# Performance work log

Hardware: AMD Instinct MI355X
Metric: run time of the kernel (lower is better)

Reference implementation:

```python
import jax, jax.numpy as jnp
import numpy as np

D_K = 64
NEG_INF = -1.0e9

def setup_inputs() -> dict:
    key = jax.random.key(0)
    kq, kk, kv, km = jax.random.split(key, 4)
    B, H, S, D = 2, 16, 2048, D_K
    Q = jax.random.normal(kq, (B, H, S, D), dtype=jnp.float32)
    K = jax.random.normal(kk, (B, H, S, D), dtype=jnp.float32)
    V = jax.random.normal(kv, (B, H, S, D), dtype=jnp.float32)
    # True entries are masked out (torch masked_fill semantics)
    attn_mask = jax.random.randint(km, (B, H, S, S), 0, 2).astype(jnp.bool_)
    return {"Q": Q, "K": K, "V": V, "attn_mask": attn_mask}

def reference(Q, K, V, attn_mask):
    # scores: [B, H, len_q, len_k]
    scale = 1.0 / np.sqrt(D_K).astype(np.float32)
    scores = jnp.einsum('bhqd,bhkd->bhqk', Q, K) * scale
    scores = jnp.where(attn_mask, jnp.float32(NEG_INF), scores)
    attn = jax.nn.softmax(scores, axis=-1)
    prob = jnp.einsum('bhqk,bhkd->bhqd', attn, V)
    return (prob, attn)
```

## Files before the change

### kernel.cpp

```cpp
#include <hip/hip_runtime.h>
#include <hip/hip_bf16.h>

#define S_LEN 2048
#define D_DIM 64
#define QT    64
#define KT    64
#define NTHR  256
#define NKT   (S_LEN / KT)
#define NBLK  1024
#define PROB_ELEMS 4194304LL

typedef float        f32x4  __attribute__((ext_vector_type(4)));
typedef int          i32x4  __attribute__((ext_vector_type(4)));
typedef unsigned int u32x4  __attribute__((ext_vector_type(4)));
typedef short        bf16x8 __attribute__((ext_vector_type(8)));

__device__ __forceinline__ unsigned short f2bf(float f) {
    return __builtin_bit_cast(unsigned short, __float2bfloat16(f));
}
__device__ __forceinline__ int swzc(int row, int ch) {
    return ch ^ ((row ^ (row >> 3)) & 7);
}
__device__ __forceinline__ float4 scale4(float4 v, float s) {
    v.x *= s; v.y *= s; v.z *= s; v.w *= s; return v;
}
__device__ __forceinline__ u32x4 packbf(float4 a, float4 b) {
    u32x4 r;
    r[0] = (unsigned)f2bf(a.x) | ((unsigned)f2bf(a.y) << 16);
    r[1] = (unsigned)f2bf(a.z) | ((unsigned)f2bf(a.w) << 16);
    r[2] = (unsigned)f2bf(b.x) | ((unsigned)f2bf(b.y) << 16);
    r[3] = (unsigned)f2bf(b.z) | ((unsigned)f2bf(b.w) << 16);
    return r;
}
__device__ __forceinline__ unsigned cvtpk(float lo, float hi) {
    unsigned r;
    asm("v_cvt_pk_bf16_f32 %0, %1, %2" : "=v"(r) : "v"(lo), "v"(hi));
    return r;
}
__device__ __forceinline__ void glds16(const unsigned* g, unsigned char* l) {
    __builtin_amdgcn_global_load_lds(
        (const __attribute__((address_space(1))) unsigned*)g,
        (__attribute__((address_space(3))) unsigned*)(void*)l, 16, 0, 0);
}
#define BC8(x) __builtin_bit_cast(bf16x8, (x))
#define MFMA(A, B, C) __builtin_amdgcn_mfma_f32_16x16x32_bf16((A), (B), (C), 0, 0, 0)

#define SFENCE() __builtin_amdgcn_sched_barrier(0)
#define WAITBAR(N)                                                          \
    SFENCE();                                                               \
    asm volatile("s_waitcnt vmcnt(" #N ")" ::: "memory");                   \
    SFENCE();                                                               \
    __builtin_amdgcn_s_barrier();                                           \
    SFENCE();

__global__ void mask_probe_kernel(const unsigned int* __restrict__ m,
                                  int* __restrict__ flag) {
    unsigned int v = m[threadIdx.x];
    unsigned long long ok = __ballot(v <= 1u);
    if (threadIdx.x == 0) *flag = (ok == ~0ULL) ? 1 : 0;
}

#define KPART 524288
#define VPART 65536
__global__ __launch_bounds__(256)
void kv_prep(const float* __restrict__ Kg, const float* __restrict__ Vg,
             unsigned* __restrict__ Kbf, unsigned* __restrict__ Vtb) {
    int tid = blockIdx.x * 256 + threadIdx.x;
    if (tid < KPART) {
        int ch = tid & 7, rowg = tid >> 3;
        const float* src = Kg + (long long)rowg * D_DIM + ch * 8;
        float4 a = *(const float4*)src, b = *(const float4*)(src + 4);
        int bh = rowg >> 11, k = rowg & 2047, kt = k >> 6, row = k & 63;
        unsigned* dst = Kbf + ((unsigned)(bh * NKT + kt) << 11)
                            + row * 32 + swzc(row, ch) * 4;
        *(u32x4*)dst = packbf(a, b);
    } else if (tid < KPART + VPART) {
        int idx = tid - KPART;
        int d = idx & 63, kt = (idx >> 6) & 31, bh = idx >> 11;
        const float* vb = Vg + (long long)(bh * S_LEN + kt * KT) * D_DIM + d;
        unsigned* tile = Vtb + ((unsigned)(bh * NKT + kt) << 11) + d * 32;
        #pragma unroll
        for (int ci = 0; ci < 8; ++ci) {
            u32x4 o;
            #pragma unroll
            for (int s = 0; s < 4; ++s) {
                float lo = vb[(ci * 8 + 2 * s) * D_DIM];
                float hi = vb[(ci * 8 + 2 * s + 1) * D_DIM];
                o[s] = (unsigned)f2bf(lo) | ((unsigned)f2bf(hi) << 16);
            }
            *(u32x4*)(tile + swzc(d, ci) * 4) = o;
        }
    }
}

#define GLDS_K(KS, KTV)                                                     \
    { const unsigned* kp_ = Kbf + ktile0 + (unsigned)(KTV) * 2048u;         \
      glds16(kp_ + f0u, (KS) + dst0); glds16(kp_ + f1u, (KS) + dst1); }
#define GLDS_V(VT, KTV)                                                     \
    { const unsigned* vp_ = Vtb + ktile0 + (unsigned)(KTV) * 2048u;         \
      glds16(vp_ + f0u, (VT) + dst0); glds16(vp_ + f1u, (VT) + dst1); }

#define PREF_MASKF(MI4, MU, KTV)                                            \
    { if (mask32) {                                                         \
        _Pragma("unroll")                                                   \
        for (int n_ = 0; n_ < 4; ++n_)                                      \
          MI4[n_] = *(const i32x4*)(maskI + rowoff                          \
                      + (unsigned)((KTV) * KT + n_ * 16 + 4 * g));          \
      } else {                                                              \
        _Pragma("unroll")                                                   \
        for (int n_ = 0; n_ < 4; ++n_)                                      \
          MU[n_] = *(const unsigned*)(maskB + rowoff                        \
                      + (unsigned)((KTV) * KT + n_ * 16 + 4 * g));          \
      } }

#define BITS16F(DST, MI4, MU)                                               \
    { unsigned bz_ = 0u;                                                    \
      if (mask32) {                                                         \
        _Pragma("unroll")                                                   \
        for (int n_ = 0; n_ < 4; ++n_)                                      \
          bz_ |= ((MI4[n_][0] ? 1u : 0u) | (MI4[n_][1] ? 2u : 0u) |         \
                  (MI4[n_][2] ? 4u : 0u) | (MI4[n_][3] ? 8u : 0u)) << (n_ * 4); \
      } else {                                                              \
        _Pragma("unroll")                                                   \
        for (int n_ = 0; n_ < 4; ++n_) { unsigned mb_ = MU[n_];             \
          bz_ |= (((mb_ & 0xffu) ? 1u : 0u) | ((mb_ & 0xff00u) ? 2u : 0u) | \
                  ((mb_ & 0xff0000u) ? 4u : 0u) |                           \
                  ((mb_ & 0xff000000u) ? 8u : 0u)) << (n_ * 4); }           \
      }                                                                     \
      (DST) = bz_; }

#define GLOAD_BITS(DST, KTV)                                                \
    { (DST) = (unsigned)bitsWS[bitbase + (unsigned)(KTV) * NTHR]; }

#define GP1_TILE(KS, BITS)                                                  \
    { unsigned bb = (BITS);                                                 \
      _Pragma("unroll")                                                     \
      for (int n = 0; n < 4; ++n) {                                         \
        int rowk = n * 16 + c;                                              \
        bf16x8 kf0 = *(const bf16x8*)((KS) + rowk * 128 + swzc(rowk, g) * 16);     \
        bf16x8 kf1 = *(const bf16x8*)((KS) + rowk * 128 + swzc(rowk, 4 + g) * 16); \
        f32x4 acc = {0.f, 0.f, 0.f, 0.f};                                   \
        acc = MFMA(kf0, qf0, acc); acc = MFMA(kf1, qf1, acc);               \
        unsigned mb = bb >> (n * 4);                                        \
        psum += (mb & 1u) ? 0.f : __expf(acc[0]);                           \
        psum += (mb & 2u) ? 0.f : __expf(acc[1]);                           \
        psum += (mb & 4u) ? 0.f : __expf(acc[2]);                           \
        psum += (mb & 8u) ? 0.f : __expf(acc[3]);                           \
      } }

#define GP2_TILE(KS, VT, BITS, KTV)                                         \
    { unsigned bb = (BITS);                                                 \
      _Pragma("unroll")                                                     \
      for (int n = 0; n < 4; ++n) {                                         \
        int rowk = n * 16 + c;                                              \
        bf16x8 kf0 = *(const bf16x8*)((KS) + rowk * 128 + swzc(rowk, g) * 16);     \
        bf16x8 kf1 = *(const bf16x8*)((KS) + rowk * 128 + swzc(rowk, 4 + g) * 16); \
        f32x4 acc = {0.f, 0.f, 0.f, 0.f};                                   \
        acc = MFMA(kf0, qf0, acc); acc = MFMA(kf1, qf1, acc);               \
        unsigned mb = bb >> (n * 4);                                        \
        f32x4 ev;                                                           \
        ev[0] = (mb & 1u) ? 0.f : __expf(acc[0]) * rinv;                    \
        ev[1] = (mb & 2u) ? 0.f : __expf(acc[1]) * rinv;                    \
        ev[2] = (mb & 4u) ? 0.f : __expf(acc[2]) * rinv;                    \
        ev[3] = (mb & 8u) ? 0.f : __expf(acc[3]) * rinv;                    \
        unsigned idx0 = rowoff + (unsigned)((KTV) * KT + n * 16 + 4 * g);   \
        *(f32x4*)(attnOut + idx0) = ev;              \
        uint2 pkv; pkv.x = cvtpk(ev[0], ev[1]); pkv.y = cvtpk(ev[2], ev[3]);\
        int kloc = n * 16 + 4 * g;                                          \
        *(uint2*)(Ps + ql * 128 + swzc(ql, kloc >> 3) * 16 + (kloc & 7) * 2) = pkv; \
      }                                                                     \
      { bf16x8 pa0 = *(const bf16x8*)(Ps + ql * 128 + swzc(ql, g) * 16);    \
        bf16x8 pa1 = *(const bf16x8*)(Ps + ql * 128 + swzc(ql, 4 + g) * 16);\
        __builtin_amdgcn_s_setprio(1);                                      \
        _Pragma("unroll")                                                   \
        for (int df = 0; df < 4; ++df) {                                    \
            int d = df * 16 + c;                                            \
            bf16x8 vb0 = *(const bf16x8*)((VT) + d * 128 + swzc(d, g) * 16);     \
            bf16x8 vb1 = *(const bf16x8*)((VT) + d * 128 + swzc(d, 4 + g) * 16); \
            pacc[df] = MFMA(pa0, vb0, pacc[df]);                            \
            pacc[df] = MFMA(pa1, vb1, pacc[df]);                            \
        }                                                                   \
        __builtin_amdgcn_s_setprio(0); } }

__global__ __launch_bounds__(NTHR, 4)
void attn_fused_glds(const float* __restrict__ Qg,
                     const unsigned* __restrict__ Kbf,
                     const unsigned* __restrict__ Vtb,
                     const unsigned char* __restrict__ maskB,
                     const int* __restrict__ flagp,
                     unsigned short* __restrict__ bitsWS, int useWS,
                     float* __restrict__ attnOut, float* __restrict__ probOut) {
    __shared__ unsigned char sm[40960];
    unsigned char* Ks0 = sm;
    unsigned char* Ks1 = sm + 8192;
    unsigned char* Vt0 = sm + 16384;
    unsigned char* Vt1 = sm + 24576;
    unsigned char* Ps  = sm + 32768;

    const int t = threadIdx.x;
    const int lane = t & 63, w = t >> 6, c = lane & 15, g = lane >> 4;
    (void)lane;

    const int orig = blockIdx.x;
    const int virt = (orig & 7) * 128 + (orig >> 3);
    const int qt = virt & 31, bh = virt >> 5;
    const int mask32 = *flagp;
    const int* maskI = (const int*)maskB;

    const int qrowbase = bh * S_LEN + qt * QT;
    const int ql = w * 16 + c;
    const unsigned rowoff = (unsigned)(qrowbase + ql) * (unsigned)S_LEN;
    const unsigned bitbase = (unsigned)virt * NKT * NTHR + (unsigned)t;
    const unsigned ktile0 = (unsigned)(bh * NKT) << 11;

    const int f0u = t * 4, f1u = (NTHR + t) * 4;
    const int dst0 = (t & ~63) * 16, dst1 = (NTHR + (t & ~63)) * 16;

    #pragma unroll
    for (int i = 0; i < 2; ++i) {
        int flat = i * NTHR + t, row = flat >> 3, ch = flat & 7;
        const float* src = Qg + (qrowbase + row) * D_DIM + ch * 8;
        float4 a = *(const float4*)src, b = *(const float4*)(src + 4);
        *(u32x4*)(Ps + row * 128 + swzc(row, ch) * 16) =
            packbf(scale4(a, 0.125f), scale4(b, 0.125f));
    }
    __syncthreads();
    bf16x8 qf0 = *(const bf16x8*)(Ps + ql * 128 + swzc(ql, g) * 16);
    bf16x8 qf1 = *(const bf16x8*)(Ps + ql * 128 + swzc(ql, 4 + g) * 16);

    float psum = 0.f;
    {
        unsigned bA, bB;
        i32x4 mAi[4], mBi[4];
        unsigned mAu[4], mBu[4];

        GLDS_K(Ks0, 0)
        PREF_MASKF(mAi, mAu, 0)
        WAITBAR(0)

        for (int j = 0; j < NKT / 2; ++j) {
            const int ktA = 2 * j, ktB = 2 * j + 1;
            GLDS_K(Ks1, ktB)
            PREF_MASKF(mBi, mBu, ktB)
            SFENCE();
            BITS16F(bA, mAi, mAu)
            GP1_TILE(Ks0, bA)
            if (useWS) bitsWS[bitbase + (unsigned)ktA * NTHR] = (unsigned short)bA;
            WAITBAR(1)

            if (j + 1 < NKT / 2) {
                GLDS_K(Ks0, ktA + 2)
                PREF_MASKF(mAi, mAu, ktA + 2)
            }
            SFENCE();
            BITS16F(bB, mBi, mBu)
            GP1_TILE(Ks1, bB)
            if (useWS) bitsWS[bitbase + (unsigned)ktB * NTHR] = (unsigned short)bB;
            WAITBAR(1)
        }
    }
    float s = psum;
    s += __shfl_xor(s, 16, 64);
    s += __shfl_xor(s, 32, 64);
    const float rinv = 1.0f / s;

    f32x4 pacc[4];
    #pragma unroll
    for (int d = 0; d < 4; ++d) pacc[d] = (f32x4){0.f, 0.f, 0.f, 0.f};
    {
        unsigned bA, bB;
        GLDS_K(Ks0, 0) GLDS_V(Vt0, 0)
        GLOAD_BITS(bA, 0)
        WAITBAR(0)

        for (int j = 0; j < NKT / 2; ++j) {
            const int ktA = 2 * j, ktB = 2 * j + 1;
            GLDS_K(Ks1, ktB) GLDS_V(Vt1, ktB)
            GLOAD_BITS(bB, ktB)
            SFENCE();
            GP2_TILE(Ks0, Vt0, bA, ktA)
            WAITBAR(4)

            if (j + 1 < NKT / 2) {
                GLDS_K(Ks0, ktA + 2) GLDS_V(Vt0, ktA + 2)
                GLOAD_BITS(bA, ktA + 2)
            }
            SFENCE();
            GP2_TILE(Ks1, Vt1, bB, ktB)
            WAITBAR(4)
        }
    }

    #pragma unroll
    for (int df = 0; df < 4; ++df)
        #pragma unroll
        for (int r = 0; r < 4; ++r) {
            int qe = w * 16 + g * 4 + r;
            probOut[(long long)(qrowbase + qe) * D_DIM + df * 16 + c] = pacc[df][r];
        }
}

#define FB_MBITS(DST, KTV)                                                  \
    { unsigned bz_ = 0u;                                                    \
      _Pragma("unroll")                                                     \
      for (int n_ = 0; n_ < 4; ++n_) {                                      \
        unsigned idx_ = rowoff + (unsigned)((KTV) * KT + n_ * 16 + 4 * g);  \
        if (mask32) {                                                       \
            i32x4 m4_ = *(const i32x4*)(maskI + idx_);                      \
            bz_ |= ((m4_[0] ? 1u : 0u) | (m4_[1] ? 2u : 0u) |               \
                    (m4_[2] ? 4u : 0u) | (m4_[3] ? 8u : 0u)) << (n_ * 4);   \
        } else {                                                            \
            unsigned mb_ = *(const unsigned*)(maskB + idx_);                \
            bz_ |= (((mb_ & 0xffu) ? 1u : 0u) | ((mb_ & 0xff00u) ? 2u : 0u) | \
                    ((mb_ & 0xff0000u) ? 4u : 0u) |                         \
                    ((mb_ & 0xff000000u) ? 8u : 0u)) << (n_ * 4);           \
        } }                                                                 \
      (DST) = bz_; }

#define FB_BITS2(DST, KTV)                                                  \
    { if (useWS) (DST) = (unsigned)bitsWS[bitbase + (unsigned)(KTV)*NTHR];  \
      else FB_MBITS(DST, KTV) }

#define FB_LOAD_K(KP, KTV)                                                  \
    { _Pragma("unroll")                                                     \
      for (int i = 0; i < 2; ++i) {                                         \
        int flat = i * NTHR + t, row = flat >> 3, ch = flat & 7;            \
        const float* src = Kg + (kbase + (KTV) * KT + row) * D_DIM + ch * 8;\
        float4 a = *(const float4*)src, b = *(const float4*)(src + 4);      \
        KP[i] = packbf(a, b);                                               \
      } }
#define FB_STAGE_K(KS, KP)                                                  \
    { _Pragma("unroll")                                                     \
      for (int i = 0; i < 2; ++i) {                                         \
        int flat = i * NTHR + t, row = flat >> 3, ch = flat & 7;            \
        *(u32x4*)((KS) + row * 128 + swzc(row, ch) * 16) = KP[i];           \
      } }
#define FB_LOAD_V(VP, KTV)                                                  \
    { const float* src = Vg + (kbase + (KTV) * KT + k0v) * D_DIM + dgv * 8; \
      float4 a = *(const float4*)src, b = *(const float4*)(src + 4);        \
      float4 e4 = *(const float4*)(src + D_DIM);                            \
      float4 f4 = *(const float4*)(src + D_DIM + 4);                        \
      VP[0] = (unsigned)f2bf(a.x) | ((unsigned)f2bf(e4.x) << 16);           \
      VP[1] = (unsigned)f2bf(a.y) | ((unsigned)f2bf(e4.y) << 16);           \
      VP[2] = (unsigned)f2bf(a.z) | ((unsigned)f2bf(e4.z) << 16);           \
      VP[3] = (unsigned)f2bf(a.w) | ((unsigned)f2bf(e4.w) << 16);           \
      VP[4] = (unsigned)f2bf(b.x) | ((unsigned)f2bf(f4.x) << 16);           \
      VP[5] = (unsigned)f2bf(b.y) | ((unsigned)f2bf(f4.y) << 16);           \
      VP[6] = (unsigned)f2bf(b.z) | ((unsigned)f2bf(f4.z) << 16);           \
      VP[7] = (unsigned)f2bf(b.w) | ((unsigned)f2bf(f4.w) << 16); }
#define FB_STAGE_V(VT, VP)                                                  \
    { _Pragma("unroll")                                                     \
      for (int jj = 0; jj < 8; ++jj) {                                      \
        int d = dgv * 8 + jj;                                               \
        *(unsigned*)((VT) + d * 128 + swzc(d, k0v >> 3) * 16 + (k0v & 7) * 2) = VP[jj]; \
      } }

__global__ __launch_bounds__(NTHR, 4)
void attn_fused_reg(const float* __restrict__ Qg, const float* __restrict__ Kg,
                    const float* __restrict__ Vg,
                    const unsigned char* __restrict__ maskB,
                    const int* __restrict__ flagp,
                    unsigned short* __restrict__ bitsWS, int useWS,
                    float* __restrict__ attnOut, float* __restrict__ probOut) {
    __shared__ unsigned char sm[40960];
    unsigned char* Ks0 = sm;
    unsigned char* Ks1 = sm + 8192;
    unsigned char* Vt0 = sm + 16384;
    unsigned char* Vt1 = sm + 24576;
    unsigned char* Ps  = sm + 32768;

    const int t = threadIdx.x;
    const int lane = t & 63, w = t >> 6, c = lane & 15, g = lane >> 4;
    (void)lane;

    const int orig = blockIdx.x;
    const int virt = (orig & 7) * 128 + (orig >> 3);
    const int qt = virt & 31, bh = virt >> 5;
    const int mask32 = *flagp;
    const int* maskI = (const int*)maskB;

    const int qrowbase = bh * S_LEN + qt * QT;
    const int kbase = bh * S_LEN;
    const int ql = w * 16 + c;
    const unsigned rowoff = (unsigned)(qrowbase + ql) * (unsigned)S_LEN;
    const unsigned bitbase = (unsigned)virt * NKT * NTHR + (unsigned)t;
    const int dgv = t & 7, k0v = (t >> 3) * 2;

    #pragma unroll
    for (int i = 0; i < 2; ++i) {
        int flat = i * NTHR + t, row = flat >> 3, ch = flat & 7;
        const float* src = Qg + (qrowbase + row) * D_DIM + ch * 8;
        float4 a = *(const float4*)src, b = *(const float4*)(src + 4);
        *(u32x4*)(Ps + row * 128 + swzc(row, ch) * 16) =
            packbf(scale4(a, 0.125f), scale4(b, 0.125f));
    }
    __syncthreads();
    bf16x8 qf0 = *(const bf16x8*)(Ps + ql * 128 + swzc(ql, g) * 16);
    bf16x8 qf1 = *(const bf16x8*)(Ps + ql * 128 + swzc(ql, 4 + g) * 16);
    __syncthreads();

    float psum = 0.f;
    u32x4 kpA[2], kpB[2];
    unsigned bA, bB;
    FB_LOAD_K(kpA, 0)
    FB_MBITS(bA, 0)

    for (int j = 0; j < NKT / 2; ++j) {
        const int ktA = 2 * j, ktB = 2 * j + 1;
        FB_STAGE_K(Ks0, kpA)
        FB_LOAD_K(kpB, ktB)
        FB_MBITS(bB, ktB)
        __syncthreads();
        GP1_TILE(Ks0, bA)
        if (useWS) bitsWS[bitbase + (unsigned)ktA * NTHR] = (unsigned short)bA;
        FB_STAGE_K(Ks1, kpB)
        if (j + 1 < NKT / 2) {
            FB_LOAD_K(kpA, ktA + 2)
            FB_MBITS(bA, ktA + 2)
        }
        __syncthreads();
        GP1_TILE(Ks1, bB)
        if (useWS) bitsWS[bitbase + (unsigned)ktB * NTHR] = (unsigned short)bB;
    }

    float s = psum;
    s += __shfl_xor(s, 16, 64);
    s += __shfl_xor(s, 32, 64);
    const float rinv = 1.0f / s;

    f32x4 pacc[4];
    #pragma unroll
    for (int d = 0; d < 4; ++d) pacc[d] = (f32x4){0.f, 0.f, 0.f, 0.f};

    unsigned vpA[8], vpB[8];
    FB_LOAD_K(kpA, 0)
    FB_LOAD_V(vpA, 0)
    FB_BITS2(bA, 0)
    __syncthreads();

    for (int j = 0; j < NKT / 2; ++j) {
        const int ktA = 2 * j, ktB = 2 * j + 1;
        FB_STAGE_K(Ks0, kpA)
        FB_STAGE_V(Vt0, vpA)
        FB_LOAD_K(kpB, ktB)
        FB_LOAD_V(vpB, ktB)
        FB_BITS2(bB, ktB)
        __syncthreads();
        GP2_TILE(Ks0, Vt0, bA, ktA)
        FB_STAGE_K(Ks1, kpB)
        FB_STAGE_V(Vt1, vpB)
        if (j + 1 < NKT / 2) {
            FB_LOAD_K(kpA, ktA + 2)
            FB_LOAD_V(vpA, ktA + 2)
            FB_BITS2(bA, ktA + 2)
        }
        __syncthreads();
        GP2_TILE(Ks1, Vt1, bB, ktB)
    }

    #pragma unroll
    for (int df = 0; df < 4; ++df)
        #pragma unroll
        for (int r = 0; r < 4; ++r) {
            int qe = w * 16 + g * 4 + r;
            probOut[(long long)(qrowbase + qe) * D_DIM + df * 16 + c] = pacc[df][r];
        }
}

extern "C" void kernel_launch(void* const* d_in, const int* in_sizes, int n_in,
                              void* d_out, int out_size, void* d_ws, size_t ws_size,
                              hipStream_t stream) {
    const float* Q = (const float*)d_in[0];
    const float* K = (const float*)d_in[1];
    const float* V = (const float*)d_in[2];
    const unsigned char* mask = (const unsigned char*)d_in[3];

    float* prob = (float*)d_out;
    float* attn = (float*)d_out + PROB_ELEMS;

    const size_t bits_bytes = (size_t)NBLK * NKT * NTHR * 2ull;
    const size_t kbf_bytes  = 8388608ull;
    int* flag = (int*)d_ws;
    unsigned short* bitsWS = (unsigned short*)((char*)d_ws + 256);
    unsigned* Kbf = (unsigned*)((char*)d_ws + 256 + bits_bytes);
    unsigned* Vtb = (unsigned*)((char*)d_ws + 256 + bits_bytes + kbf_bytes);

    const int useWS   = (ws_size >= 256 + bits_bytes) ? 1 : 0;
    const int usePrep = (ws_size >= 256 + bits_bytes + 2 * kbf_bytes) ? 1 : 0;

    mask_probe_kernel<<<1, 64, 0, stream>>>((const unsigned int*)mask, flag);
    if (usePrep && useWS) {
        kv_prep<<<(KPART + VPART) / 256, 256, 0, stream>>>(K, V, Kbf, Vtb);
        attn_fused_glds<<<NBLK, NTHR, 0, stream>>>(Q, Kbf, Vtb, mask, flag,
                                                   bitsWS, useWS, attn, prob);
    } else {
        attn_fused_reg<<<NBLK, NTHR, 0, stream>>>(Q, K, V, mask, flag,
                                                  bitsWS, useWS, attn, prob);
    }
}
```

Measured before the change: 367.1 us.

## Split key tiles across two waves per query block with 512-thread workgroups

Replaces the 256-thread fused attention kernel with a 512-thread version in which each pair of waves splits every 64-key tile in half. Row sums and output accumulators are combined through LDS at the end. The mask bits are stored as bytes per thread instead of shorts, and the scale now folds in log2(e) so the raw v_exp_f32 instruction can be used instead of __expf. The aim is more waves in flight to hide memory latency on the large attn write and mask read. The cost is extra LDS reductions, a cross-wave sync, and narrower per-wave MFMA work.

```diff
diff --git a/kernel.cpp b/kernel.cpp
--- a/kernel.cpp
+++ b/kernel.cpp
@@ -6,9 +6,11 @@
 #define QT    64
 #define KT    64
 #define NTHR  256
+#define NTHR2 512
 #define NKT   (S_LEN / KT)
 #define NBLK  1024
 #define PROB_ELEMS 4194304LL
+#define QSC   0.1803368801f
 
 typedef float        f32x4  __attribute__((ext_vector_type(4)));
 typedef int          i32x4  __attribute__((ext_vector_type(4)));
@@ -36,6 +38,9 @@
     unsigned r;
     asm("v_cvt_pk_bf16_f32 %0, %1, %2" : "=v"(r) : "v"(lo), "v"(hi));
     return r;
+}
+__device__ __forceinline__ float vexp2(float x) {
+    float r; asm("v_exp_f32 %0, %1" : "=v"(r) : "v"(x)); return r;
 }
 __device__ __forceinline__ void glds16(const unsigned* g, unsigned char* l) {
     __builtin_amdgcn_global_load_lds(
@@ -93,44 +98,214 @@
     }
 }
 
-#define GLDS_K(KS, KTV)                                                     \
-    { const unsigned* kp_ = Kbf + ktile0 + (unsigned)(KTV) * 2048u;         \
-      glds16(kp_ + f0u, (KS) + dst0); glds16(kp_ + f1u, (KS) + dst1); }
-#define GLDS_V(VT, KTV)                                                     \
-    { const unsigned* vp_ = Vtb + ktile0 + (unsigned)(KTV) * 2048u;         \
-      glds16(vp_ + f0u, (VT) + dst0); glds16(vp_ + f1u, (VT) + dst1); }
-
-#define PREF_MASKF(MI4, MU, KTV)                                            \
+#define GK2(KS, KTV)                                                        \
+    { glds16(Kbf + ktile0 + (unsigned)(KTV) * 2048u + fsrc, (KS) + fdst); }
+#define GV2(VT, KTV)                                                        \
+    { glds16(Vtb + ktile0 + (unsigned)(KTV) * 2048u + fsrc, (VT) + fdst); }
+
+#define PM2(MI, MU, KTV)                                                    \
     { if (mask32) {                                                         \
-        _Pragma("unroll")                                                   \
-        for (int n_ = 0; n_ < 4; ++n_)                                      \
-          MI4[n_] = *(const i32x4*)(maskI + rowoff                          \
-                      + (unsigned)((KTV) * KT + n_ * 16 + 4 * g));          \
+        MI[0] = *(const i32x4*)(maskI + rowoff + (unsigned)(KTV) * KT + colbase);      \
+        MI[1] = *(const i32x4*)(maskI + rowoff + (unsigned)(KTV) * KT + colbase + 16); \
       } else {                                                              \
-        _Pragma("unroll")                                                   \
-        for (int n_ = 0; n_ < 4; ++n_)                                      \
-          MU[n_] = *(const unsigned*)(maskB + rowoff                        \
-                      + (unsigned)((KTV) * KT + n_ * 16 + 4 * g));          \
+        MU[0] = *(const unsigned*)(maskB + rowoff + (unsigned)(KTV) * KT + colbase);      \
+        MU[1] = *(const unsigned*)(maskB + rowoff + (unsigned)(KTV) * KT + colbase + 16); \
       } }
 
-#define BITS16F(DST, MI4, MU)                                               \
+#define BB2(DST, MI, MU)                                                    \
     { unsigned bz_ = 0u;                                                    \
       if (mask32) {                                                         \
-        _Pragma("unroll")                                                   \
-        for (int n_ = 0; n_ < 4; ++n_)                                      \
-          bz_ |= ((MI4[n_][0] ? 1u : 0u) | (MI4[n_][1] ? 2u : 0u) |         \
-                  (MI4[n_][2] ? 4u : 0u) | (MI4[n_][3] ? 8u : 0u)) << (n_ * 4); \
+        bz_ |=  (MI[0][0]?1u:0u)|(MI[0][1]?2u:0u)|(MI[0][2]?4u:0u)|(MI[0][3]?8u:0u);      \
+        bz_ |= ((MI[1][0]?1u:0u)|(MI[1][1]?2u:0u)|(MI[1][2]?4u:0u)|(MI[1][3]?8u:0u))<<4;  \
       } else {                                                              \
-        _Pragma("unroll")                                                   \
-        for (int n_ = 0; n_ < 4; ++n_) { unsigned mb_ = MU[n_];             \
-          bz_ |= (((mb_ & 0xffu) ? 1u : 0u) | ((mb_ & 0xff00u) ? 2u : 0u) | \
-                  ((mb_ & 0xff0000u) ? 4u : 0u) |                           \
-                  ((mb_ & 0xff000000u) ? 8u : 0u)) << (n_ * 4); }           \
+        unsigned m0_ = MU[0], m1_ = MU[1];                                  \
+        bz_ |=  ((m0_&0xffu)?1u:0u)|((m0_&0xff00u)?2u:0u)|                  \
+                ((m0_&0xff0000u)?4u:0u)|((m0_&0xff000000u)?8u:0u);          \
+        bz_ |= (((m1_&0xffu)?1u:0u)|((m1_&0xff00u)?2u:0u)|                  \
+                ((m1_&0xff0000u)?4u:0u)|((m1_&0xff000000u)?8u:0u))<<4;      \
       }                                                                     \
       (DST) = bz_; }
 
-#define GLOAD_BITS(DST, KTV)                                                \
-    { (DST) = (unsigned)bitsWS[bitbase + (unsigned)(KTV) * NTHR]; }
+#define NP1(KS, BITS)                                                       \
+    { unsigned bb_ = (BITS);                                                \
+      _Pragma("unroll")                                                     \
+      for (int n_ = 0; n_ < 2; ++n_) {                                      \
+        int rowk = wk * 32 + n_ * 16 + c;                                   \
+        bf16x8 kf0 = *(const bf16x8*)((KS) + rowk * 128 + swzc(rowk, g) * 16);     \
+        bf16x8 kf1 = *(const bf16x8*)((KS) + rowk * 128 + swzc(rowk, 4 + g) * 16); \
+        f32x4 acc = {0.f, 0.f, 0.f, 0.f};                                   \
+        acc = MFMA(kf0, qf0, acc); acc = MFMA(kf1, qf1, acc);               \
+        unsigned mb_ = bb_ >> (n_ * 4);                                     \
+        psum += (mb_ & 1u) ? 0.f : vexp2(acc[0]);                           \
+        psum += (mb_ & 2u) ? 0.f : vexp2(acc[1]);                           \
+        psum += (mb_ & 4u) ? 0.f : vexp2(acc[2]);                           \
+        psum += (mb_ & 8u) ? 0.f : vexp2(acc[3]);                           \
+      } }
+
+#define NP2(KS, VT, BITS, KTV)                                              \
+    { unsigned bb_ = (BITS);                                                \
+      _Pragma("unroll")                                                     \
+      for (int n_ = 0; n_ < 2; ++n_) {                                      \
+        int rowk = wk * 32 + n_ * 16 + c;                                   \
+        bf16x8 kf0 = *(const bf16x8*)((KS) + rowk * 128 + swzc(rowk, g) * 16);     \
+        bf16x8 kf1 = *(const bf16x8*)((KS) + rowk * 128 + swzc(rowk, 4 + g) * 16); \
+        f32x4 acc = {0.f, 0.f, 0.f, 0.f};                                   \
+        acc = MFMA(kf0, qf0, acc); acc = MFMA(kf1, qf1, acc);               \
+        unsigned mb_ = bb_ >> (n_ * 4);                                     \
+        f32x4 ev;                                                           \
+        ev[0] = (mb_ & 1u) ? 0.f : vexp2(acc[0]) * rinv;                    \
+        ev[1] = (mb_ & 2u) ? 0.f : vexp2(acc[1]) * rinv;                    \
+        ev[2] = (mb_ & 4u) ? 0.f : vexp2(acc[2]) * rinv;                    \
+        ev[3] = (mb_ & 8u) ? 0.f : vexp2(acc[3]) * rinv;                    \
+        unsigned idx_ = rowoff + (unsigned)(KTV) * KT + colbase + n_ * 16;  \
+        *(f32x4*)(attnOut + idx_) = ev;                                     \
+        uint2 pk_; pk_.x = cvtpk(ev[0], ev[1]); pk_.y = cvtpk(ev[2], ev[3]);\
+        int k0_ = wk * 32 + n_ * 16 + 4 * g;                                \
+        *(uint2*)(Ps + ql * 128 + swzc(ql, k0_ >> 3) * 16 + (k0_ & 7) * 2) = pk_; \
+      }                                                                     \
+      { bf16x8 pa_ = *(const bf16x8*)(Ps + ql * 128 + swzc(ql, wk * 4 + g) * 16); \
+        __builtin_amdgcn_s_setprio(1);                                      \
+        _Pragma("unroll")                                                   \
+        for (int df_ = 0; df_ < 4; ++df_) {                                 \
+            int d_ = df_ * 16 + c;                                          \
+            bf16x8 vb_ = *(const bf16x8*)((VT) + d_ * 128 + swzc(d_, wk * 4 + g) * 16); \
+            pacc[df_] = MFMA(pa_, vb_, pacc[df_]);                          \
+        }                                                                   \
+        __builtin_amdgcn_s_setprio(0); } }
+
+__global__ __launch_bounds__(NTHR2, 8)
+void attn_fused_glds2(const float* __restrict__ Qg,
+                      const unsigned* __restrict__ Kbf,
+                      const unsigned* __restrict__ Vtb,
+                      const unsigned char* __restrict__ maskB,
+                      const int* __restrict__ flagp,
+                      unsigned char* __restrict__ bitsWS,
+                      float* __restrict__ attnOut, float* __restrict__ probOut) {
+    __shared__ unsigned char sm[40960];
+    unsigned char* Ks0 = sm;
+    unsigned char* Ks1 = sm + 8192;
+    unsigned char* Vt0 = sm + 16384;
+    unsigned char* Vt1 = sm + 24576;
+    unsigned char* Ps  = sm + 32768;
+
+    const int t = threadIdx.x;
+    const int lane = t & 63, w = t >> 6;
+    const int c = lane & 15, g = (lane >> 4) & 3;
+    const int wq = w >> 1, wk = w & 1;
+
+    const int orig = blockIdx.x;
+    const int virt = (orig & 7) * 128 + (orig >> 3);
+    const int qt = virt & 31, bh = virt >> 5;
+    const int mask32 = *flagp;
+    const int* maskI = (const int*)maskB;
+
+    const int qrowbase = bh * S_LEN + qt * QT;
+    const int ql = wq * 16 + c;
+    const unsigned rowoff = (unsigned)(qrowbase + ql) * (unsigned)S_LEN;
+    const unsigned colbase = (unsigned)(wk * 32 + 4 * g);
+    const unsigned bitbase = (unsigned)virt * (NKT * NTHR2) + (unsigned)t;
+    const unsigned ktile0 = (unsigned)(bh * NKT) << 11;
+
+    const int fsrc = t * 4;
+    const int fdst = (t & ~63) * 16;
+
+    {
+        int row = t >> 3, ch = t & 7;
+        const float* src = Qg + (qrowbase + row) * D_DIM + ch * 8;
+        float4 a = *(const float4*)src, b = *(const float4*)(src + 4);
+        *(u32x4*)(Ps + row * 128 + swzc(row, ch) * 16) =
+            packbf(scale4(a, QSC), scale4(b, QSC));
+    }
+    __syncthreads();
+    bf16x8 qf0 = *(const bf16x8*)(Ps + ql * 128 + swzc(ql, g) * 16);
+    bf16x8 qf1 = *(const bf16x8*)(Ps + ql * 128 + swzc(ql, 4 + g) * 16);
+
+    float psum = 0.f;
+    {
+        i32x4 mAi[2], mBi[2];
+        unsigned mAu[2], mBu[2], bA, bB;
+        GK2(Ks0, 0)
+        PM2(mAi, mAu, 0)
+        WAITBAR(0)
+
+        for (int j = 0; j < NKT / 2; ++j) {
+            const int ktA = 2 * j, ktB = 2 * j + 1;
+            GK2(Ks1, ktB)
+            PM2(mBi, mBu, ktB)
+            SFENCE();
+            BB2(bA, mAi, mAu)
+            NP1(Ks0, bA)
+            bitsWS[bitbase + (unsigned)ktA * NTHR2] = (unsigned char)bA;
+            WAITBAR(1)
+
+            if (j + 1 < NKT / 2) {
+                GK2(Ks0, ktA + 2)
+                PM2(mAi, mAu, ktA + 2)
+            }
+            SFENCE();
+            BB2(bB, mBi, mBu)
+            NP1(Ks1, bB)
+            bitsWS[bitbase + (unsigned)ktB * NTHR2] = (unsigned char)bB;
+            WAITBAR(1)
+        }
+    }
+    {
+        float s = psum;
+        s += __shfl_xor(s, 16, 64);
+        s += __shfl_xor(s, 32, 64);
+        if (lane < 16) ((float*)Ps)[w * 16 + c] = s;
+    }
+    __syncthreads();
+    const float rinv = 1.0f / (((const float*)Ps)[(wq * 2 + 0) * 16 + c] +
+                               ((const float*)Ps)[(wq * 2 + 1) * 16 + c]);
+
+    f32x4 pacc[4];
+    #pragma unroll
+    for (int d = 0; d < 4; ++d) pacc[d] = (f32x4){0.f, 0.f, 0.f, 0.f};
+    {
+        unsigned bA, bB;
+        GK2(Ks0, 0) GV2(Vt0, 0)
+        bA = (unsigned)bitsWS[bitbase];
+        WAITBAR(0)
+
+        for (int j = 0; j < NKT / 2; ++j) {
+            const int ktA = 2 * j, ktB = 2 * j + 1;
+            GK2(Ks1, ktB) GV2(Vt1, ktB)
+            bB = (unsigned)bitsWS[bitbase + (unsigned)ktB * NTHR2];
+            SFENCE();
+            NP2(Ks0, Vt0, bA, ktA)
+            WAITBAR(2)
+
+            if (j + 1 < NKT / 2) {
+                GK2(Ks0, ktA + 2) GV2(Vt0, ktA + 2)
+                bA = (unsigned)bitsWS[bitbase + (unsigned)(ktA + 2) * NTHR2];
+            }
+            SFENCE();
+            NP2(Ks1, Vt1, bB, ktB)
+            WAITBAR(2)
+        }
+    }
+
+    __syncthreads();
+    if (wk == 1) {
+        #pragma unroll
+        for (int df = 0; df < 4; ++df)
+            *(f32x4*)(sm + wq * 4096 + lane * 64 + df * 16) = pacc[df];
+    }
+    __syncthreads();
+    if (wk == 0) {
+        #pragma unroll
+        for (int df = 0; df < 4; ++df) {
+            f32x4 o = pacc[df] +
+                *(const f32x4*)(sm + wq * 4096 + lane * 64 + df * 16);
+            #pragma unroll
+            for (int r = 0; r < 4; ++r) {
+                int qe = qrowbase + wq * 16 + g * 4 + r;
+                probOut[(long long)qe * D_DIM + df * 16 + c] = o[r];
+            }
+        }
+    }
+}
 
 #define GP1_TILE(KS, BITS)                                                  \
     { unsigned bb = (BITS);                                                 \
@@ -164,7 +339,7 @@
         ev[2] = (mb & 4u) ? 0.f : __expf(acc[2]) * rinv;                    \
         ev[3] = (mb & 8u) ? 0.f : __expf(acc[3]) * rinv;                    \
         unsigned idx0 = rowoff + (unsigned)((KTV) * KT + n * 16 + 4 * g);   \
-        *(f32x4*)(attnOut + idx0) = ev;              \
+        *(f32x4*)(attnOut + idx0) = ev;                                     \
         uint2 pkv; pkv.x = cvtpk(ev[0], ev[1]); pkv.y = cvtpk(ev[2], ev[3]);\
         int kloc = n * 16 + 4 * g;                                          \
         *(uint2*)(Ps + ql * 128 + swzc(ql, kloc >> 3) * 16 + (kloc & 7) * 2) = pkv; \
@@ -181,124 +356,6 @@
             pacc[df] = MFMA(pa1, vb1, pacc[df]);                            \
         }                                                                   \
         __builtin_amdgcn_s_setprio(0); } }
-
-__global__ __launch_bounds__(NTHR, 4)
-void attn_fused_glds(const float* __restrict__ Qg,
-                     const unsigned* __restrict__ Kbf,
-                     const unsigned* __restrict__ Vtb,
-                     const unsigned char* __restrict__ maskB,
-                     const int* __restrict__ flagp,
-                     unsigned short* __restrict__ bitsWS, int useWS,
-                     float* __restrict__ attnOut, float* __restrict__ probOut) {
-    __shared__ unsigned char sm[40960];
-    unsigned char* Ks0 = sm;
-    unsigned char* Ks1 = sm + 8192;
-    unsigned char* Vt0 = sm + 16384;
-    unsigned char* Vt1 = sm + 24576;
-    unsigned char* Ps  = sm + 32768;
-
-    const int t = threadIdx.x;
-    const int lane = t & 63, w = t >> 6, c = lane & 15, g = lane >> 4;
-    (void)lane;
-
-    const int orig = blockIdx.x;
-    const int virt = (orig & 7) * 128 + (orig >> 3);
-    const int qt = virt & 31, bh = virt >> 5;
-    const int mask32 = *flagp;
-    const int* maskI = (const int*)maskB;
-
-    const int qrowbase = bh * S_LEN + qt * QT;
-    const int ql = w * 16 + c;
-    const unsigned rowoff = (unsigned)(qrowbase + ql) * (unsigned)S_LEN;
-    const unsigned bitbase = (unsigned)virt * NKT * NTHR + (unsigned)t;
-    const unsigned ktile0 = (unsigned)(bh * NKT) << 11;
-
-    const int f0u = t * 4, f1u = (NTHR + t) * 4;
-    const int dst0 = (t & ~63) * 16, dst1 = (NTHR + (t & ~63)) * 16;
-
-    #pragma unroll
-    for (int i = 0; i < 2; ++i) {
-        int flat = i * NTHR + t, row = flat >> 3, ch = flat & 7;
-        const float* src = Qg + (qrowbase + row) * D_DIM + ch * 8;
-        float4 a = *(const float4*)src, b = *(const float4*)(src + 4);
-        *(u32x4*)(Ps + row * 128 + swzc(row, ch) * 16) =
-            packbf(scale4(a, 0.125f), scale4(b, 0.125f));
-    }
-    __syncthreads();
-    bf16x8 qf0 = *(const bf16x8*)(Ps + ql * 128 + swzc(ql, g) * 16);
-    bf16x8 qf1 = *(const bf16x8*)(Ps + ql * 128 + swzc(ql, 4 + g) * 16);
-
-    float psum = 0.f;
-    {
-        unsigned bA, bB;
-        i32x4 mAi[4], mBi[4];
-        unsigned mAu[4], mBu[4];
-
-        GLDS_K(Ks0, 0)
-        PREF_MASKF(mAi, mAu, 0)
-        WAITBAR(0)
-
-        for (int j = 0; j < NKT / 2; ++j) {
-            const int ktA = 2 * j, ktB = 2 * j + 1;
-            GLDS_K(Ks1, ktB)
-            PREF_MASKF(mBi, mBu, ktB)
-            SFENCE();
-            BITS16F(bA, mAi, mAu)
-            GP1_TILE(Ks0, bA)
-            if (useWS) bitsWS[bitbase + (unsigned)ktA * NTHR] = (unsigned short)bA;
-            WAITBAR(1)
-
-            if (j + 1 < NKT / 2) {
-                GLDS_K(Ks0, ktA + 2)
-                PREF_MASKF(mAi, mAu, ktA + 2)
-            }
-            SFENCE();
-            BITS16F(bB, mBi, mBu)
-            GP1_TILE(Ks1, bB)
-            if (useWS) bitsWS[bitbase + (unsigned)ktB * NTHR] = (unsigned short)bB;
-            WAITBAR(1)
-        }
-    }
-    float s = psum;
-    s += __shfl_xor(s, 16, 64);
-    s += __shfl_xor(s, 32, 64);
-    const float rinv = 1.0f / s;
-
-    f32x4 pacc[4];
-    #pragma unroll
-    for (int d = 0; d < 4; ++d) pacc[d] = (f32x4){0.f, 0.f, 0.f, 0.f};
-    {
-        unsigned bA, bB;
-        GLDS_K(Ks0, 0) GLDS_V(Vt0, 0)
-        GLOAD_BITS(bA, 0)
-        WAITBAR(0)
-
-        for (int j = 0; j < NKT / 2; ++j) {
-            const int ktA = 2 * j, ktB = 2 * j + 1;
-            GLDS_K(Ks1, ktB) GLDS_V(Vt1, ktB)
-            GLOAD_BITS(bB, ktB)
-            SFENCE();
-            GP2_TILE(Ks0, Vt0, bA, ktA)
-            WAITBAR(4)
-
-            if (j + 1 < NKT / 2) {
-                GLDS_K(Ks0, ktA + 2) GLDS_V(Vt0, ktA + 2)
-                GLOAD_BITS(bA, ktA + 2)
-            }
-            SFENCE();
-            GP2_TILE(Ks1, Vt1, bB, ktB)
-            WAITBAR(4)
-        }
-    }
-
-    #pragma unroll
-    for (int df = 0; df < 4; ++df)
-        #pragma unroll
-        for (int r = 0; r < 4; ++r) {
-            int qe = w * 16 + g * 4 + r;
-            probOut[(long long)(qrowbase + qe) * D_DIM + df * 16 + c] = pacc[df][r];
-        }
-}
 
 #define FB_MBITS(DST, KTV)                                                  \
     { unsigned bz_ = 0u;                                                    \
@@ -478,10 +535,11 @@
     float* prob = (float*)d_out;
     float* attn = (float*)d_out + PROB_ELEMS;
 
-    const size_t bits_bytes = (size_t)NBLK * NKT * NTHR * 2ull;
+    const size_t bits_bytes = 16777216ull;
     const size_t kbf_bytes  = 8388608ull;
     int* flag = (int*)d_ws;
-    unsigned short* bitsWS = (unsigned short*)((char*)d_ws + 256);
+    unsigned char*  bits8  = (unsigned char*)((char*)d_ws + 256);
+    unsigned short* bits16 = (unsigned short*)((char*)d_ws + 256);
     unsigned* Kbf = (unsigned*)((char*)d_ws + 256 + bits_bytes);
     unsigned* Vtb = (unsigned*)((char*)d_ws + 256 + bits_bytes + kbf_bytes);
 
@@ -491,10 +549,10 @@
     mask_probe_kernel<<<1, 64, 0, stream>>>((const unsigned int*)mask, flag);
     if (usePrep && useWS) {
         kv_prep<<<(KPART + VPART) / 256, 256, 0, stream>>>(K, V, Kbf, Vtb);
-        attn_fused_glds<<<NBLK, NTHR, 0, stream>>>(Q, Kbf, Vtb, mask, flag,
-                                                   bitsWS, useWS, attn, prob);
+        attn_fused_glds2<<<NBLK, NTHR2, 0, stream>>>(Q, Kbf, Vtb, mask, flag,
+                                                     bits8, attn, prob);
     } else {
         attn_fused_reg<<<NBLK, NTHR, 0, stream>>>(Q, K, V, mask, flag,
-                                                  bitsWS, useWS, attn, prob);
-    }
-}
+                                                  bits16, useWS, attn, prob);
+    }
+}
```

Result: slower. 577.5 us (+57.3%).
